# Kernel optimization log

Measured on AMD Instinct MI355X. Metric: run time of the kernel, lower is better.

Reference implementation:

```python
import jax, jax.numpy as jnp
import numpy as np

D_MODEL = 512; D_STATE = 64; D_CONV = 4; HEADDIM = 64
D_INNER = 2 * D_MODEL              # expand=2
NHEADS = D_INNER // HEADDIM        # 16
CONV_DIM = D_INNER + 2 * D_STATE   # 1152
D_IN_PROJ = 2 * D_INNER + 2 * D_STATE + NHEADS  # 2192
BATCH, SEQ = 4, 1024
EPS = 1e-5


def rmsnorm(x, w):
    return x * jax.lax.rsqrt(jnp.mean(x * x, axis=-1, keepdims=True) + EPS) * w


def mamba2(u, in_w, conv_w, conv_b, dt_bias, A_log, D, gnorm_w, out_w):
    b, l, _ = u.shape
    zxbcdt = u @ in_w.T                                  # [b,l,D_IN_PROJ]
    z = zxbcdt[..., :D_INNER]
    xBC = zxbcdt[..., D_INNER:D_INNER + CONV_DIM]
    dt = jax.nn.softplus(zxbcdt[..., -NHEADS:] + dt_bias)  # [b,l,h]
    # causal depthwise conv1d (kernel D_CONV, left pad) + silu
    pad = jnp.pad(xBC, ((0, 0), (D_CONV - 1, 0), (0, 0)))
    acc = conv_b
    for k in range(D_CONV):
        acc = acc + pad[:, k:k + l, :] * conv_w[:, k]
    xBC = jax.nn.silu(acc)
    x = xBC[..., :D_INNER].reshape(b, l, NHEADS, HEADDIM)
    Bm = xBC[..., D_INNER:D_INNER + D_STATE]             # [b,l,n]
    Cm = xBC[..., D_INNER + D_STATE:]                    # [b,l,n]
    A = -jnp.exp(A_log)                                  # [h]
    decay = jnp.exp(dt * A)                              # [b,l,h]
    dtx = dt[..., None] * x                              # [b,l,h,p]

    def step(h, inp):
        dec, dx, Bt, Ct = inp
        h = h * dec[:, :, None, None] + dx[..., None] * Bt[:, None, None, :]
        y = jnp.einsum('bhpn,bn->bhp', h, Ct)
        return h, y

    h0 = jnp.zeros((b, NHEADS, HEADDIM, D_STATE), u.dtype)
    _, ys = jax.lax.scan(step, h0, (decay.transpose(1, 0, 2),
                                    dtx.transpose(1, 0, 2, 3),
                                    Bm.transpose(1, 0, 2),
                                    Cm.transpose(1, 0, 2)))
    y = ys.transpose(1, 0, 2, 3) + x * D[None, None, :, None]  # [b,l,h,p]
    y = y.reshape(b, l, D_INNER)
    y = rmsnorm(y * jax.nn.silu(z), gnorm_w)             # gated RMSNorm
    return y @ out_w.T


def setup_inputs() -> dict:
    key = jax.random.key(0)
    ks = iter(jax.random.split(key, 32))
    def rn(shape, scale=0.02):
        return jax.random.normal(next(ks), shape, dtype=jnp.float32) * scale
    inp = {
        'x': jax.random.normal(next(ks), (BATCH, SEQ, D_MODEL), dtype=jnp.float32),
        'norm_w': jnp.ones((D_MODEL,), jnp.float32),
    }
    for p in ('f', 'b'):
        inp[p + '_in_w'] = rn((D_IN_PROJ, D_MODEL))
        inp[p + '_conv_w'] = rn((CONV_DIM, D_CONV), 0.1)
        inp[p + '_conv_b'] = jnp.zeros((CONV_DIM,), jnp.float32)
        inp[p + '_dt_bias'] = rn((NHEADS,), 0.5)
        inp[p + '_A_log'] = jnp.log(jnp.arange(1, NHEADS + 1, dtype=jnp.float32))
        inp[p + '_D'] = jnp.ones((NHEADS,), jnp.float32)
        inp[p + '_gnorm_w'] = jnp.ones((D_INNER,), jnp.float32)
        inp[p + '_out_w'] = rn((D_MODEL, D_INNER))
    inp['proj_w'] = rn((D_MODEL, 2 * D_MODEL))
    return inp


def reference(x, norm_w,
              f_in_w, f_conv_w, f_conv_b, f_dt_bias, f_A_log, f_D, f_gnorm_w, f_out_w,
              b_in_w, b_conv_w, b_conv_b, b_dt_bias, b_A_log, b_D, b_gnorm_w, b_out_w,
              proj_w):
    h = rmsnorm(x, norm_w)
    fo = mamba2(h, f_in_w, f_conv_w, f_conv_b, f_dt_bias, f_A_log, f_D, f_gnorm_w, f_out_w)
    bo = jnp.flip(mamba2(jnp.flip(h, 1), b_in_w, b_conv_w, b_conv_b, b_dt_bias,
                         b_A_log, b_D, b_gnorm_w, b_out_w), 1)
    return x + jnp.concatenate([fo, bo], axis=-1) @ proj_w.T
```

## Files before the change

kernel.cpp:

```cpp
#include <hip/hip_runtime.h>
#include <math.h>

typedef unsigned short u16;
typedef __bf16  bf16x8 __attribute__((ext_vector_type(8)));
typedef float   f32x4  __attribute__((ext_vector_type(4)));
typedef unsigned short u16x8 __attribute__((ext_vector_type(8)));

#define SEQ 1024
#define MR  4096
#define DIP 2192
#define DI  1024
#define NH  16
#define CD  1152
#define NCH 32
#define CT  32
#define NIN (DIP*512)
#define NOUT (512*1024)
#define ZROW 4384

__device__ __forceinline__ u16 f2bf(float f) {
  union { float f; unsigned u; } v; v.f = f;
  unsigned r = v.u + 0x7FFFu + ((v.u >> 16) & 1u);
  return (u16)(r >> 16);
}
__device__ __forceinline__ float bf2f(u16 h) {
  union { unsigned u; float f; } v; v.u = ((unsigned)h) << 16; return v.f;
}
__device__ __forceinline__ void splitbf(float v, u16& h, u16& l) {
  h = f2bf(v); l = f2bf(v - bf2f(h));
}
__device__ __forceinline__ float sigm(float x){ return 1.f/(1.f+__expf(-x)); }

__device__ __forceinline__ unsigned packbf(float v) {
  u16 hh, ll; splitbf(v, hh, ll);
  return (unsigned)hh | ((unsigned)ll << 16);
}
__device__ __forceinline__ float unpackf(unsigned w) {
  return bf2f((u16)w) + bf2f((u16)(w >> 16));
}

__device__ __forceinline__ void unpack8(const unsigned* p, bf16x8& H, bf16x8& L) {
  uint4 a = *(const uint4*)p, b = *(const uint4*)(p+4);
  u16x8 hu, lu;
  hu[0]=(u16)a.x; lu[0]=(u16)(a.x>>16);
  hu[1]=(u16)a.y; lu[1]=(u16)(a.y>>16);
  hu[2]=(u16)a.z; lu[2]=(u16)(a.z>>16);
  hu[3]=(u16)a.w; lu[3]=(u16)(a.w>>16);
  hu[4]=(u16)b.x; lu[4]=(u16)(b.x>>16);
  hu[5]=(u16)b.y; lu[5]=(u16)(b.y>>16);
  hu[6]=(u16)b.z; lu[6]=(u16)(b.z>>16);
  hu[7]=(u16)b.w; lu[7]=(u16)(b.w>>16);
  H = __builtin_bit_cast(bf16x8, hu);
  L = __builtin_bit_cast(bf16x8, lu);
}
__device__ __forceinline__ void unpack8s(const unsigned* p, int stride, bf16x8& H, bf16x8& L) {
  u16x8 hu, lu;
  #pragma unroll
  for (int jj=0;jj<8;jj++){ unsigned w = p[(size_t)jj*stride]; hu[jj]=(u16)w; lu[jj]=(u16)(w>>16); }
  H = __builtin_bit_cast(bf16x8, hu);
  L = __builtin_bit_cast(bf16x8, lu);
}

__device__ __forceinline__ void gl16(const u16* g, u16* l) {
  __builtin_amdgcn_global_load_lds((const __attribute__((address_space(1))) void*)g,
                                   (__attribute__((address_space(3))) void*)l,
                                   16, 0, 0);
}

__global__ __launch_bounds__(256) void cast_all(
  const float* __restrict__ f_in, const float* __restrict__ b_in,
  const float* __restrict__ f_out, const float* __restrict__ b_out,
  const float* __restrict__ proj,
  u16* __restrict__ H, u16* __restrict__ L, unsigned* __restrict__ wpk)
{
  int i = blockIdx.x*256 + threadIdx.x;
  constexpr int TOT = 2*NIN + 3*NOUT;
  if (i >= TOT) return;
  float v;
  if (i < NIN)               v = f_in[i];
  else if (i < 2*NIN)        v = b_in[i-NIN];
  else if (i < 2*NIN+NOUT)   v = f_out[i-2*NIN];
  else if (i < 2*NIN+2*NOUT) v = b_out[i-2*NIN-NOUT];
  else                       v = proj[i-2*NIN-2*NOUT];
  if (i < 2*NIN) {
    u16 hh, ll; splitbf(v, hh, ll);
    H[i] = hh; L[i] = ll;
  } else {
    wpk[i - 2*NIN] = packbf(v);
  }
}

__global__ __launch_bounds__(256) void wcomb(
  const unsigned* __restrict__ wpk,
  u16* __restrict__ Wch, u16* __restrict__ Wcl)
{
  int d = blockIdx.z;
  int o0 = blockIdx.x*64, p0 = blockIdx.y*128;
  int wv = threadIdx.x>>6, lane = threadIdx.x&63;
  int quad = lane>>4, l16 = lane&15;
  const unsigned* owp = wpk + (size_t)d*NOUT;
  const unsigned* pjp = wpk + 2*(size_t)NOUT;
  int pc = p0 + wv*32;
  f32x4 acc[4][2] = {};
  for (int kt=0; kt<512; kt+=32) {
    bf16x8 ahf[4], alf[4], bhf[2], blf[2];
    #pragma unroll
    for (int ia=0; ia<4; ia++)
      unpack8(pjp + (size_t)(o0 + 16*ia + l16)*1024 + d*512 + kt + quad*8, ahf[ia], alf[ia]);
    #pragma unroll
    for (int jb=0; jb<2; jb++)
      unpack8s(owp + (size_t)(kt + quad*8)*1024 + pc + 16*jb + l16, 1024, bhf[jb], blf[jb]);
    #pragma unroll
    for (int ia=0; ia<4; ia++)
      #pragma unroll
      for (int jb=0; jb<2; jb++) {
        f32x4 t = __builtin_amdgcn_mfma_f32_16x16x32_bf16(ahf[ia], blf[jb], acc[ia][jb], 0,0,0);
        t       = __builtin_amdgcn_mfma_f32_16x16x32_bf16(alf[ia], bhf[jb], t,           0,0,0);
        acc[ia][jb] = __builtin_amdgcn_mfma_f32_16x16x32_bf16(ahf[ia], bhf[jb], t,       0,0,0);
      }
  }
  #pragma unroll
  for (int ia=0; ia<4; ia++)
  #pragma unroll
  for (int jb=0; jb<2; jb++)
  #pragma unroll
  for (int r=0; r<4; r++) {
    int o = o0 + 16*ia + quad*4 + r;
    int p = pc + 16*jb + l16;
    u16 hh, ll; splitbf(acc[ia][jb][r], hh, ll);
    Wch[(size_t)d*NOUT + (size_t)o*1024 + p] = hh;
    Wcl[(size_t)d*NOUT + (size_t)o*1024 + p] = ll;
  }
}

__global__ __launch_bounds__(256) void rmsnorm_x(const float* __restrict__ x,
                                                 const float* __restrict__ w,
                                                 u16* __restrict__ hbh,
                                                 u16* __restrict__ hbl){
  int m = blockIdx.x, tid = threadIdx.x;
  const float* xr = x + (size_t)m*512;
  float2 v = *(const float2*)&xr[tid*2];
  float ss = v.x*v.x + v.y*v.y;
  #pragma unroll
  for (int off=32; off; off>>=1) ss += __shfl_xor(ss, off, 64);
  __shared__ float red[4];
  if ((tid&63)==0) red[tid>>6] = ss;
  __syncthreads();
  float total = red[0]+red[1]+red[2]+red[3];
  float rs = rsqrtf(total*(1.f/512.f) + 1e-5f);
  float2 w2 = *(const float2*)&w[tid*2];
  u16 h0,l0,h1,l1;
  splitbf(v.x*rs*w2.x, h0, l0);
  splitbf(v.y*rs*w2.y, h1, l1);
  *(unsigned*)&hbh[(size_t)m*512 + tid*2] = (unsigned)h0 | ((unsigned)h1<<16);
  *(unsigned*)&hbl[(size_t)m*512 + tid*2] = (unsigned)l0 | ((unsigned)l1<<16);
}

__global__ __launch_bounds__(256) void gemm_in(
    const u16* __restrict__ Ah, const u16* __restrict__ Al,
    const u16* __restrict__ Wh, const u16* __restrict__ Wl,
    float* __restrict__ C0)
{
  constexpr int K = 512;
  constexpr int N = DIP;
  __shared__ __align__(16) u16 sAh[128*32];
  __shared__ __align__(16) u16 sAl[128*32];
  __shared__ __align__(16) u16 sBh[128*32];
  __shared__ __align__(16) u16 sBl[128*32];
  const int tid = threadIdx.x;
  const int dir = blockIdx.z;
  const int m0 = blockIdx.x * 128;
  const int n0 = blockIdx.y * 128;
  const int lane = tid & 63;
  const int wid  = tid >> 6;
  const u16* wh_p = Wh + (size_t)dir*NIN;
  const u16* wl_p = Wl + (size_t)dir*NIN;
  const int j0 = wid, j1 = wid + 4;
  const int cp = lane & 3;
  auto goff = [&](int j, bool isB)->size_t {
    int row = 16*j + (lane>>2);
    int s = (row>>1) & 3;
    int kc = (cp ^ s) * 8;
    int grow;
    if (!isB) {
      grow = m0 + row;
      if (dir) grow = (grow & ~1023) + (1023 - (grow & 1023));
    } else {
      grow = n0 + row;
      if (grow >= N) grow = N-1;
    }
    return (size_t)grow*K + kc;
  };
  const size_t a0 = goff(j0,false), a1 = goff(j1,false);
  const size_t b0 = goff(j0,true),  b1 = goff(j1,true);
  const int wm = (wid & 1) * 64;
  const int wn = (wid >> 1) * 64;
  const int quad = lane >> 4;
  const int l16  = lane & 15;
  const int qx = quad ^ ((l16>>1)&3);
  const int baseA = ((wm + l16)*4 + qx)*8;
  const int baseB = ((wn + l16)*4 + qx)*8;
  f32x4 acc[4][4] = {};
  for (int kt = 0; kt < K; kt += 32) {
    __syncthreads();
    gl16(Ah + a0 + kt, &sAh[j0*512]);  gl16(Ah + a1 + kt, &sAh[j1*512]);
    gl16(Al + a0 + kt, &sAl[j0*512]);  gl16(Al + a1 + kt, &sAl[j1*512]);
    gl16(wh_p + b0 + kt, &sBh[j0*512]);  gl16(wh_p + b1 + kt, &sBh[j1*512]);
    gl16(wl_p + b0 + kt, &sBl[j0*512]);  gl16(wl_p + b1 + kt, &sBl[j1*512]);
    __syncthreads();
    bf16x8 ah[4], al[4], bh[4], bl[4];
    #pragma unroll
    for (int i=0;i<4;i++) {
      ah[i] = *(const bf16x8*)&sAh[baseA + i*512];
      al[i] = *(const bf16x8*)&sAl[baseA + i*512];
    }
    #pragma unroll
    for (int j=0;j<4;j++) {
      bh[j] = *(const bf16x8*)&sBh[baseB + j*512];
      bl[j] = *(const bf16x8*)&sBl[baseB + j*512];
    }
    #pragma unroll
    for (int i=0;i<4;i++)
      #pragma unroll
      for (int j=0;j<4;j++) {
        f32x4 t = __builtin_amdgcn_mfma_f32_16x16x32_bf16(ah[i], bl[j], acc[i][j], 0,0,0);
        t       = __builtin_amdgcn_mfma_f32_16x16x32_bf16(al[i], bh[j], t,         0,0,0);
        acc[i][j] = __builtin_amdgcn_mfma_f32_16x16x32_bf16(ah[i], bh[j], t,       0,0,0);
      }
  }
  #pragma unroll
  for (int i=0;i<4;i++)
  #pragma unroll
  for (int j=0;j<4;j++)
  #pragma unroll
  for (int r=0;r<4;r++) {
    int mo = m0 + wm + i*16 + quad*4 + r;
    int no = n0 + wn + j*16 + l16;
    if (no < N) C0[((size_t)dir*MR + mo)*DIP + no] = acc[i][j][r];
  }
}

__global__ __launch_bounds__(512) void gemm_final(
    const u16* __restrict__ zt, const u16* __restrict__ Wch, const u16* __restrict__ Wcl,
    const float* __restrict__ X0, float* __restrict__ out)
{
  __shared__ __align__(16) u16 sAh[64*32];
  __shared__ __align__(16) u16 sAl[64*32];
  __shared__ __align__(16) u16 sBh[128*32];
  __shared__ __align__(16) u16 sBl[128*32];
  const int tid = threadIdx.x;
  const int lane = tid & 63, wid = tid >> 6;
  const int m0 = blockIdx.x * 64, n0 = blockIdx.y * 128;
  const int cp = lane & 3;
  const int quad = lane >> 4, l16 = lane & 15;
  const int wm = (wid & 1) * 32;
  const int wn = (wid >> 1) * 32;
  const int qx = quad ^ ((l16>>1)&3);
  const int baseA = ((wm + l16)*4 + qx)*8;
  const int baseB = ((wn + l16)*4 + qx)*8;
  f32x4 acc[2][2] = {};
  const int jb0 = (wid-4)*2, jb1 = jb0+1;
  for (int dir=0; dir<2; ++dir) {
    size_t aoff=0, boff0=0, boff1=0;
    if (wid < 4) {
      int row = 16*wid + (lane>>2);
      int s = (row>>1) & 3;
      int kc = (cp ^ s) * 8;
      int grow = m0 + row;
      if (dir) grow = (grow & ~1023) + (1023 - (grow & 1023));
      aoff = (size_t)(dir*MR + grow)*ZROW + kc;
    } else {
      int row0 = 16*jb0 + (lane>>2);
      int s0 = (row0>>1) & 3;
      boff0 = (size_t)dir*NOUT + (size_t)(n0 + row0)*1024 + (cp ^ s0)*8;
      int row1 = 16*jb1 + (lane>>2);
      int s1 = (row1>>1) & 3;
      boff1 = (size_t)dir*NOUT + (size_t)(n0 + row1)*1024 + (cp ^ s1)*8;
    }
    for (int kt = 0; kt < 1024; kt += 32) {
      __syncthreads();
      if (wid < 4) {
        gl16(zt + 2048 + aoff + kt, &sAh[wid*512]);
        gl16(zt + 3072 + aoff + kt, &sAl[wid*512]);
      } else {
        gl16(Wch + boff0 + kt, &sBh[jb0*512]);
        gl16(Wch + boff1 + kt, &sBh[jb1*512]);
        gl16(Wcl + boff0 + kt, &sBl[jb0*512]);
        gl16(Wcl + boff1 + kt, &sBl[jb1*512]);
      }
      __syncthreads();
      bf16x8 ah[2], al[2], bh[2], bl[2];
      #pragma unroll
      for (int i=0;i<2;i++) {
        ah[i] = *(const bf16x8*)&sAh[baseA + i*512];
        al[i] = *(const bf16x8*)&sAl[baseA + i*512];
      }
      #pragma unroll
      for (int j=0;j<2;j++) {
        bh[j] = *(const bf16x8*)&sBh[baseB + j*512];
        bl[j] = *(const bf16x8*)&sBl[baseB + j*512];
      }
      #pragma unroll
      for (int i=0;i<2;i++)
        #pragma unroll
        for (int j=0;j<2;j++) {
          f32x4 t = __builtin_amdgcn_mfma_f32_16x16x32_bf16(ah[i], bl[j], acc[i][j], 0,0,0);
          t       = __builtin_amdgcn_mfma_f32_16x16x32_bf16(al[i], bh[j], t,         0,0,0);
          acc[i][j] = __builtin_amdgcn_mfma_f32_16x16x32_bf16(ah[i], bh[j], t,       0,0,0);
        }
    }
  }
  #pragma unroll
  for (int i=0;i<2;i++)
  #pragma unroll
  for (int j=0;j<2;j++)
  #pragma unroll
  for (int r=0;r<4;r++) {
    int mo = m0 + wm + 16*i + quad*4 + r;
    int no = n0 + wn + 16*j + l16;
    out[(size_t)mo*512 + no] = acc[i][j][r] + X0[(size_t)mo*512 + no];
  }
}

__global__ __launch_bounds__(320) void conv_dt(
  const float* __restrict__ Z,
  const float* __restrict__ f_cw, const float* __restrict__ f_cb,
  const float* __restrict__ b_cw, const float* __restrict__ b_cb,
  const float* __restrict__ f_dtb, const float* __restrict__ b_dtb,
  unsigned* __restrict__ xconv,
  unsigned* __restrict__ Bc, unsigned* __restrict__ Cc,
  float* __restrict__ dtq)
{
  int bm = blockIdx.x;
  int dir = bm >> 12;
  int t = bm & 1023;
  const float* cw  = dir ? b_cw : f_cw;
  const float* cb  = dir ? b_cb : f_cb;
  const float* dtb = dir ? b_dtb : f_dtb;
  int tid = threadIdx.x;
  if (tid < 288) {
    int c0 = tid*4;
    const float* zbase = Z + (size_t)(bm-3)*DIP + 1024 + c0;
    float4 w0 = *(const float4*)&cw[c0*4];
    float4 w1 = *(const float4*)&cw[(c0+1)*4];
    float4 w2 = *(const float4*)&cw[(c0+2)*4];
    float4 w3 = *(const float4*)&cw[(c0+3)*4];
    float4 z0 = {0,0,0,0}, z1 = {0,0,0,0}, z2 = {0,0,0,0};
    float4 z3 = *(const float4*)(zbase + 3*(size_t)DIP);
    if (t >= 3) {
      z0 = *(const float4*)(zbase);
      z1 = *(const float4*)(zbase + (size_t)DIP);
      z2 = *(const float4*)(zbase + 2*(size_t)DIP);
    } else {
      if (t >= 1) z2 = *(const float4*)(zbase + 2*(size_t)DIP);
      if (t >= 2) z1 = *(const float4*)(zbase + (size_t)DIP);
    }
    float4 a = *(const float4*)&cb[c0];
    a.x += z0.x*w0.x + z1.x*w0.y + z2.x*w0.z + z3.x*w0.w;
    a.y += z0.y*w1.x + z1.y*w1.y + z2.y*w1.z + z3.y*w1.w;
    a.z += z0.z*w2.x + z1.z*w2.y + z2.z*w2.z + z3.z*w2.w;
    a.w += z0.w*w3.x + z1.w*w3.y + z2.w*w3.z + z3.w*w3.w;
    float4 v;
    v.x = a.x * sigm(a.x); v.y = a.y * sigm(a.y);
    v.z = a.z * sigm(a.z); v.w = a.w * sigm(a.w);
    uint4 pv;
    pv.x = packbf(v.x); pv.y = packbf(v.y);
    pv.z = packbf(v.z); pv.w = packbf(v.w);
    if (c0 < 1024)      *(uint4*)&xconv[(size_t)bm*DI + c0] = pv;
    else if (c0 < 1088) *(uint4*)&Bc[(size_t)bm*64 + (c0-1024)] = pv;
    else                *(uint4*)&Cc[(size_t)bm*64 + (c0-1088)] = pv;
  }
  if (tid < NH) {
    float dtraw = Z[(size_t)bm*DIP + 2176 + tid] + dtb[tid];
    float dt = (dtraw > 20.f) ? dtraw : log1pf(__expf(dtraw));
    dtq[(size_t)bm*NH + tid] = dt;
  }
}

__global__ __launch_bounds__(256) void scan_mfma(
  const float* __restrict__ dtq, const unsigned* __restrict__ xconv,
  const unsigned* __restrict__ Bc, const unsigned* __restrict__ Cc,
  const float* __restrict__ f_Al, const float* __restrict__ b_Al,
  float* __restrict__ yraw, float* __restrict__ cumdec, float* __restrict__ S)
{
  __shared__ __align__(16) u16 sMh[4][32*40];
  __shared__ __align__(16) u16 sMl[4][32*40];
  __shared__ float scum[4][32];
  __shared__ float sdt[4][32];
  int bx = blockIdx.x;
  int hq = bx & 3, chunk = (bx>>2)&(NCH-1), dirb = bx>>7;
  int w = threadIdx.x >> 6, lane = threadIdx.x & 63;
  int h = hq*4 + w;
  int base_row = dirb*1024 + chunk*CT;
  const int quad = lane >> 4, l16 = lane & 15;
  const float* Al = (dirb >= 4) ? b_Al : f_Al;
  float A = -__expf(Al[h]);
  float dtl = 0.f, cum = 0.f;
  if (lane < 32) { dtl = dtq[(size_t)(base_row + lane)*16 + h]; cum = dtl; }
  #pragma unroll
  for (int off=1; off<32; off<<=1) {
    int src = (lane >= off) ? lane-off : lane;
    float o = __shfl(cum, src);
    if (lane >= off && lane < 32) cum += o;
  }
  if (lane < 32) {
    sdt[w][lane]  = dtl;
    scum[w][lane] = cum;
    cumdec[(size_t)(base_row + lane)*16 + h] = __expf(A*cum);
  }
  bf16x8 chf[2][2], clf[2][2], bhf[2][2], blf[2][2];
  #pragma unroll
  for (int i=0;i<2;i++)
  #pragma unroll
  for (int kk=0;kk<2;kk++) {
    unpack8(Cc + (size_t)(base_row + 16*i + l16)*64 + kk*32 + quad*8, chf[i][kk], clf[i][kk]);
    unpack8(Bc + (size_t)(base_row + 16*i + l16)*64 + kk*32 + quad*8, bhf[i][kk], blf[i][kk]);
  }
  f32x4 g[2][2];
  __builtin_amdgcn_s_setprio(1);
  #pragma unroll
  for (int i=0;i<2;i++)
  #pragma unroll
  for (int j=0;j<2;j++) {
    f32x4 acc = {};
    #pragma unroll
    for (int kk=0;kk<2;kk++) {
      acc = __builtin_amdgcn_mfma_f32_16x16x32_bf16(chf[i][kk], blf[j][kk], acc, 0,0,0);
      acc = __builtin_amdgcn_mfma_f32_16x16x32_bf16(clf[i][kk], bhf[j][kk], acc, 0,0,0);
      acc = __builtin_amdgcn_mfma_f32_16x16x32_bf16(chf[i][kk], bhf[j][kk], acc, 0,0,0);
    }
    g[i][j] = acc;
  }
  __builtin_amdgcn_s_setprio(0);
  float ctt[2][4];
  #pragma unroll
  for (int i=0;i<2;i++)
  #pragma unroll
  for (int r=0;r<4;r++) ctt[i][r] = scum[w][16*i + quad*4 + r];
  #pragma unroll
  for (int j=0;j<2;j++) {
    int s = 16*j + l16;
    float cts = scum[w][s];
    float dts = sdt[w][s];
    #pragma unroll
    for (int i=0;i<2;i++)
    #pragma unroll
    for (int r=0;r<4;r++) {
      int t = 16*i + quad*4 + r;
      float mv = (s <= t) ? g[i][j][r] * __expf(A*(ctt[i][r]-cts)) * dts : 0.f;
      u16 hh, ll; splitbf(mv, hh, ll);
      sMh[w][t*40 + s] = hh;
      sMl[w][t*40 + s] = ll;
    }
  }
  bf16x8 xhf[4], xlf[4];
  const unsigned* xp = xconv + (size_t)(base_row + quad*8)*1024 + h*64 + l16;
  #pragma unroll
  for (int jp=0;jp<4;jp++) unpack8s(xp + 16*jp, 1024, xhf[jp], xlf[jp]);
  bf16x8 mhf[2], mlf[2];
  #pragma unroll
  for (int i=0;i<2;i++) {
    mhf[i] = *(const bf16x8*)&sMh[w][(16*i + l16)*40 + quad*8];
    mlf[i] = *(const bf16x8*)&sMl[w][(16*i + l16)*40 + quad*8];
  }
  __builtin_amdgcn_s_setprio(1);
  #pragma unroll
  for (int i=0;i<2;i++)
  #pragma unroll
  for (int jp=0;jp<4;jp++) {
    f32x4 acc = {};
    acc = __builtin_amdgcn_mfma_f32_16x16x32_bf16(mhf[i], xlf[jp], acc, 0,0,0);
    acc = __builtin_amdgcn_mfma_f32_16x16x32_bf16(mlf[i], xhf[jp], acc, 0,0,0);
    acc = __builtin_amdgcn_mfma_f32_16x16x32_bf16(mhf[i], xhf[jp], acc, 0,0,0);
    #pragma unroll
    for (int r=0;r<4;r++)
      yraw[(size_t)(base_row + 16*i + quad*4 + r)*1024 + h*64 + 16*jp + l16] = acc[r];
  }
  __builtin_amdgcn_s_setprio(0);
  float wv[8];
  float ct31 = scum[w][31];
  #pragma unroll
  for (int jj=0;jj<8;jj++) {
    int s = quad*8 + jj;
    wv[jj] = sdt[w][s] * __expf(A*(ct31 - scum[w][s]));
  }
  bf16x8 wbh[4], wbl[4];
  #pragma unroll
  for (int j2=0;j2<4;j2++) {
    u16x8 hu, lu; u16 hh, ll;
    #pragma unroll
    for (int jj=0;jj<8;jj++) {
      float b = unpackf(Bc[(size_t)(base_row + quad*8 + jj)*64 + 16*j2 + l16]);
      splitbf(wv[jj]*b, hh, ll); hu[jj]=hh; lu[jj]=ll;
    }
    wbh[j2] = __builtin_bit_cast(bf16x8, hu);
    wbl[j2] = __builtin_bit_cast(bf16x8, lu);
  }
  size_t inst = ((size_t)(dirb*16+h)*NCH + chunk)*4096;
  __builtin_amdgcn_s_setprio(1);
  #pragma unroll
  for (int mp=0;mp<4;mp++)
  #pragma unroll
  for (int j2=0;j2<4;j2++) {
    f32x4 acc = {};
    acc = __builtin_amdgcn_mfma_f32_16x16x32_bf16(xhf[mp], wbl[j2], acc, 0,0,0);
    acc = __builtin_amdgcn_mfma_f32_16x16x32_bf16(xlf[mp], wbh[j2], acc, 0,0,0);
    acc = __builtin_amdgcn_mfma_f32_16x16x32_bf16(xhf[mp], wbh[j2], acc, 0,0,0);
    #pragma unroll
    for (int r=0;r<4;r++)
      S[inst + (size_t)(16*mp + quad*4 + r)*64 + 16*j2 + l16] = acc[r];
  }
  __builtin_amdgcn_s_setprio(0);
}

__global__ __launch_bounds__(256) void scan_comb(
  const float* __restrict__ cumdec, float* __restrict__ S)
{
  int ih = blockIdx.x >> 4;
  int sub = blockIdx.x & 15;
  int dirb = ih >> 4, h = ih & 15;
  int elem = sub*256 + threadIdx.x;
  size_t base = (size_t)ih*NCH*4096 + elem;
  float hr = 0.f;
  for (int c=0;c<NCH;c++) {
    float P = cumdec[((size_t)(dirb*1024 + c*CT + CT-1))*16 + h];
    float s = S[base + c*4096];
    S[base + c*4096] = __builtin_bit_cast(float, packbf(hr));
    hr = fmaf(hr, P, s);
  }
}

__global__ __launch_bounds__(1024) void scan_y2_gate(
  const unsigned* __restrict__ Cc, const float* __restrict__ cumdec,
  const float* __restrict__ S, const float* __restrict__ yraw,
  const unsigned* __restrict__ xconv, const float* Z, u16* zt,
  const float* __restrict__ f_D, const float* __restrict__ b_D,
  const float* __restrict__ f_gw, const float* __restrict__ b_gw)
{
  __shared__ float vbuf[32][1028];
  __shared__ float red[32][17];
  __shared__ float rsb[32];
  int bx = blockIdx.x;
  int chunk = bx & (NCH-1), dirb = bx >> 5;
  int w = threadIdx.x >> 6, lane = threadIdx.x & 63;
  int h = w;
  int dir = dirb >> 2;
  int row0 = dirb*1024 + chunk*CT;
  const int quad = lane>>4, l16 = lane&15;
  const float* Dp  = dir ? b_D  : f_D;
  const float* gwp = dir ? b_gw : f_gw;
  float Dv = Dp[h];

  f32x4 acc[2][4] = {};
  float at[2][4] = {};
  if (chunk > 0) {
    size_t inst = ((size_t)(dirb*16+h)*NCH + chunk)*4096;
    #pragma unroll
    for (int i=0;i<2;i++)
    #pragma unroll
    for (int r=0;r<4;r++)
      at[i][r] = cumdec[(size_t)(row0 + 16*i + quad*4 + r)*16 + h];
    bf16x8 chf[2][2], clf[2][2];
    #pragma unroll
    for (int i=0;i<2;i++)
    #pragma unroll
    for (int kk=0;kk<2;kk++)
      unpack8(Cc + (size_t)(row0 + 16*i + l16)*64 + kk*32 + quad*8, chf[i][kk], clf[i][kk]);
    const unsigned* Sp = (const unsigned*)S;
    __builtin_amdgcn_s_setprio(1);
    #pragma unroll
    for (int j=0;j<4;j++) {
      bf16x8 hhf[2], hlf[2];
      #pragma unroll
      for (int kk=0;kk<2;kk++)
        unpack8(Sp + inst + (size_t)(16*j + l16)*64 + kk*32 + quad*8, hhf[kk], hlf[kk]);
      #pragma unroll
      for (int i=0;i<2;i++) {
        f32x4 a2 = acc[i][j];
        #pragma unroll
        for (int kk=0;kk<2;kk++) {
          a2 = __builtin_amdgcn_mfma_f32_16x16x32_bf16(chf[i][kk], hlf[kk], a2, 0,0,0);
          a2 = __builtin_amdgcn_mfma_f32_16x16x32_bf16(clf[i][kk], hhf[kk], a2, 0,0,0);
          a2 = __builtin_amdgcn_mfma_f32_16x16x32_bf16(chf[i][kk], hhf[kk], a2, 0,0,0);
        }
        acc[i][j] = a2;
      }
    }
    __builtin_amdgcn_s_setprio(0);
  }
  float pss[2][4] = {};
  #pragma unroll
  for (int i=0;i<2;i++)
  #pragma unroll
  for (int r=0;r<4;r++) {
    int t = 16*i + quad*4 + r;
    size_t g = (size_t)(row0 + t);
    #pragma unroll
    for (int j=0;j<4;j++) {
      int c = h*64 + 16*j + l16;
      float yv = yraw[g*1024 + c];
      float xv = unpackf(xconv[g*1024 + c]);
      float zv = Z[g*DIP + c];
      float v = (yv + xv*Dv + at[i][r]*acc[i][j][r]) * (zv * sigm(zv));
      vbuf[t][c] = v;
      pss[i][r] += v*v;
    }
  }
  #pragma unroll
  for (int i=0;i<2;i++)
  #pragma unroll
  for (int r=0;r<4;r++) {
    float s2 = pss[i][r];
    s2 += __shfl_xor(s2, 1, 64);
    s2 += __shfl_xor(s2, 2, 64);
    s2 += __shfl_xor(s2, 4, 64);
    s2 += __shfl_xor(s2, 8, 64);
    if (l16 == 0) red[16*i + quad*4 + r][w] = s2;
  }
  __syncthreads();
  if (threadIdx.x < 32) {
    int t = threadIdx.x;
    float tot = 0.f;
    #pragma unroll
    for (int ww=0; ww<16; ww++) tot += red[t][ww];
    rsb[t] = rsqrtf(tot*(1.f/1024.f) + 1e-5f);
  }
  __syncthreads();
  #pragma unroll
  for (int i=0;i<2;i++)
  #pragma unroll
  for (int r=0;r<4;r++) {
    int t = 16*i + quad*4 + r;
    size_t g = (size_t)(row0 + t);
    float rs = rsb[t];
    #pragma unroll
    for (int j=0;j<4;j++) {
      int c = h*64 + 16*j + l16;
      float o = vbuf[t][c] * rs * gwp[c];
      u16 hh, ll; splitbf(o, hh, ll);
      zt[g*ZROW + 2048 + c] = hh;
      zt[g*ZROW + 3072 + c] = ll;
    }
  }
}

extern "C" void kernel_launch(void* const* d_in, const int* in_sizes, int n_in,
                              void* d_out, int out_size, void* d_ws, size_t ws_size,
                              hipStream_t stream)
{
  const float* x        = (const float*)d_in[0];
  const float* norm_w   = (const float*)d_in[1];
  const float* f_in_w   = (const float*)d_in[2];
  const float* f_conv_w = (const float*)d_in[3];
  const float* f_conv_b = (const float*)d_in[4];
  const float* f_dt_bias= (const float*)d_in[5];
  const float* f_A_log  = (const float*)d_in[6];
  const float* f_D      = (const float*)d_in[7];
  const float* f_gw     = (const float*)d_in[8];
  const float* f_out_w  = (const float*)d_in[9];
  const float* b_in_w   = (const float*)d_in[10];
  const float* b_conv_w = (const float*)d_in[11];
  const float* b_conv_b = (const float*)d_in[12];
  const float* b_dt_bias= (const float*)d_in[13];
  const float* b_A_log  = (const float*)d_in[14];
  const float* b_D      = (const float*)d_in[15];
  const float* b_gw     = (const float*)d_in[16];
  const float* b_out_w  = (const float*)d_in[17];
  const float* proj_w   = (const float*)d_in[18];

  char* ws = (char*)d_ws;
  size_t off = 0;
  auto alloc = [&](size_t bytes)->char* {
    char* p = ws + off; off = (off + bytes + 255) & ~(size_t)255; return p;
  };
  u16*   hbh   = (u16*)  alloc((size_t)MR*512*2);
  u16*   hbl   = (u16*)  alloc((size_t)MR*512*2);
  u16*   wH    = (u16*)  alloc(2*(size_t)NIN*2);
  u16*   wL    = (u16*)  alloc(2*(size_t)NIN*2);
  unsigned* wpk = (unsigned*)alloc(3*(size_t)NOUT*4);
  u16*   Wch   = (u16*)  alloc(2*(size_t)NOUT*2);
  u16*   Wcl   = (u16*)  alloc(2*(size_t)NOUT*2);
  float* Z     = (float*)alloc(2*(size_t)MR*DIP*4);
  unsigned* xconv = (unsigned*)alloc(2*(size_t)MR*DI*4);
  unsigned* Bc    = (unsigned*)alloc(2*(size_t)MR*64*4);
  unsigned* Cc    = (unsigned*)alloc(2*(size_t)MR*64*4);
  float* dtq   = (float*)alloc(2*(size_t)MR*NH*4);
  float* cumdec= (float*)alloc(2*(size_t)MR*NH*4);
  float* S     = (float*)alloc((size_t)4096*4096*4);
  float* yraw  = (float*)alloc(2*(size_t)MR*DI*4);
  u16* wih = wH;  u16* wil = wL;

  constexpr int TOT = 2*NIN + 3*NOUT;
  cast_all<<<(TOT+255)/256,256,0,stream>>>(f_in_w, b_in_w, f_out_w, b_out_w, proj_w,
                                           wH, wL, wpk);
  wcomb<<<dim3(8,8,2),256,0,stream>>>(wpk, Wch, Wcl);

  rmsnorm_x<<<MR,256,0,stream>>>(x, norm_w, hbh, hbl);
  gemm_in<<<dim3(32,18,2),256,0,stream>>>(hbh, hbl, wih, wil, Z);
  conv_dt<<<2*MR,320,0,stream>>>(Z, f_conv_w, f_conv_b, b_conv_w, b_conv_b,
                                 f_dt_bias, b_dt_bias, xconv, Bc, Cc, dtq);
  scan_mfma<<<1024,256,0,stream>>>(dtq, xconv, Bc, Cc, f_A_log, b_A_log,
                                   yraw, cumdec, S);
  scan_comb<<<2048,256,0,stream>>>(cumdec, S);
  scan_y2_gate<<<256,1024,0,stream>>>(Cc, cumdec, S, yraw, xconv, Z, (u16*)Z,
                                      f_D, b_D, f_gw, b_gw);
  gemm_final<<<dim3(64,4),512,0,stream>>>((u16*)Z, Wch, Wcl, x, (float*)d_out);
}
```

Baseline: 380.4 us.

## Split final GEMM K-loop across directions into separate blocks with add kernel

The final projection GEMM used to loop over both scan directions inside one 512-thread block. It now launches one 256-thread block per direction via blockIdx.z, doubling the grid from 256 to 512 blocks. The forward direction writes output plus residual, and the backward direction writes a partial into a reused yraw buffer. A new elementwise kernel then adds the two. This raises parallelism and occupancy for a small grid, at the cost of an extra launch and an extra 8MB read/write pass.

```diff
diff --git a/kernel.cpp b/kernel.cpp
--- a/kernel.cpp
+++ b/kernel.cpp
@@ -240,86 +240,97 @@
   }
 }
 
-__global__ __launch_bounds__(512) void gemm_final(
+__global__ __launch_bounds__(256) void gemm_final(
     const u16* __restrict__ zt, const u16* __restrict__ Wch, const u16* __restrict__ Wcl,
-    const float* __restrict__ X0, float* __restrict__ out)
-{
+    const float* __restrict__ X0, float* __restrict__ out, float* __restrict__ Pb)
+{
+  constexpr int K = 1024;
   __shared__ __align__(16) u16 sAh[64*32];
   __shared__ __align__(16) u16 sAl[64*32];
   __shared__ __align__(16) u16 sBh[128*32];
   __shared__ __align__(16) u16 sBl[128*32];
   const int tid = threadIdx.x;
-  const int lane = tid & 63, wid = tid >> 6;
-  const int m0 = blockIdx.x * 64, n0 = blockIdx.y * 128;
+  const int dir = blockIdx.z;
+  const int m0 = blockIdx.x * 64;
+  const int n0 = blockIdx.y * 128;
+  const int lane = tid & 63;
+  const int wid  = tid >> 6;
+  const u16* ah_p = zt + 2048 + (size_t)dir*MR*ZROW;
+  const u16* al_p = zt + 3072 + (size_t)dir*MR*ZROW;
+  const u16* wh_p = Wch + (size_t)dir*NOUT;
+  const u16* wl_p = Wcl + (size_t)dir*NOUT;
   const int cp = lane & 3;
-  const int quad = lane >> 4, l16 = lane & 15;
-  const int wm = (wid & 1) * 32;
-  const int wn = (wid >> 1) * 32;
+  auto goffA = [&](int j)->size_t {
+    int row = 16*j + (lane>>2);
+    int s = (row>>1) & 3;
+    int kc = (cp ^ s) * 8;
+    int grow = m0 + row;
+    if (dir) grow = (grow & ~1023) + (1023 - (grow & 1023));
+    return (size_t)grow*ZROW + kc;
+  };
+  auto goffB = [&](int j)->size_t {
+    int row = 16*j + (lane>>2);
+    int s = (row>>1) & 3;
+    int kc = (cp ^ s) * 8;
+    return (size_t)(n0 + row)*1024 + kc;
+  };
+  const size_t a0 = goffA(wid);
+  const size_t b0 = goffB(wid), b1 = goffB(wid+4);
+  const int quad = lane >> 4;
+  const int l16  = lane & 15;
   const int qx = quad ^ ((l16>>1)&3);
-  const int baseA = ((wm + l16)*4 + qx)*8;
-  const int baseB = ((wn + l16)*4 + qx)*8;
-  f32x4 acc[2][2] = {};
-  const int jb0 = (wid-4)*2, jb1 = jb0+1;
-  for (int dir=0; dir<2; ++dir) {
-    size_t aoff=0, boff0=0, boff1=0;
-    if (wid < 4) {
-      int row = 16*wid + (lane>>2);
-      int s = (row>>1) & 3;
-      int kc = (cp ^ s) * 8;
-      int grow = m0 + row;
-      if (dir) grow = (grow & ~1023) + (1023 - (grow & 1023));
-      aoff = (size_t)(dir*MR + grow)*ZROW + kc;
-    } else {
-      int row0 = 16*jb0 + (lane>>2);
-      int s0 = (row0>>1) & 3;
-      boff0 = (size_t)dir*NOUT + (size_t)(n0 + row0)*1024 + (cp ^ s0)*8;
-      int row1 = 16*jb1 + (lane>>2);
-      int s1 = (row1>>1) & 3;
-      boff1 = (size_t)dir*NOUT + (size_t)(n0 + row1)*1024 + (cp ^ s1)*8;
-    }
-    for (int kt = 0; kt < 1024; kt += 32) {
-      __syncthreads();
-      if (wid < 4) {
-        gl16(zt + 2048 + aoff + kt, &sAh[wid*512]);
-        gl16(zt + 3072 + aoff + kt, &sAl[wid*512]);
-      } else {
-        gl16(Wch + boff0 + kt, &sBh[jb0*512]);
-        gl16(Wch + boff1 + kt, &sBh[jb1*512]);
-        gl16(Wcl + boff0 + kt, &sBl[jb0*512]);
-        gl16(Wcl + boff1 + kt, &sBl[jb1*512]);
-      }
-      __syncthreads();
-      bf16x8 ah[2], al[2], bh[2], bl[2];
-      #pragma unroll
-      for (int i=0;i<2;i++) {
-        ah[i] = *(const bf16x8*)&sAh[baseA + i*512];
-        al[i] = *(const bf16x8*)&sAl[baseA + i*512];
-      }
+  const int baseA = (l16*4 + qx)*8;
+  const int baseB = ((wid*32 + l16)*4 + qx)*8;
+  f32x4 acc[4][2] = {};
+  for (int kt = 0; kt < K; kt += 32) {
+    __syncthreads();
+    gl16(ah_p + a0 + kt, &sAh[wid*512]);
+    gl16(al_p + a0 + kt, &sAl[wid*512]);
+    gl16(wh_p + b0 + kt, &sBh[wid*512]);  gl16(wh_p + b1 + kt, &sBh[(wid+4)*512]);
+    gl16(wl_p + b0 + kt, &sBl[wid*512]);  gl16(wl_p + b1 + kt, &sBl[(wid+4)*512]);
+    __syncthreads();
+    bf16x8 ah[4], al[4], bh[2], bl[2];
+    #pragma unroll
+    for (int i=0;i<4;i++) {
+      ah[i] = *(const bf16x8*)&sAh[baseA + i*512];
+      al[i] = *(const bf16x8*)&sAl[baseA + i*512];
+    }
+    #pragma unroll
+    for (int j=0;j<2;j++) {
+      bh[j] = *(const bf16x8*)&sBh[baseB + j*512];
+      bl[j] = *(const bf16x8*)&sBl[baseB + j*512];
+    }
+    #pragma unroll
+    for (int i=0;i<4;i++)
       #pragma unroll
       for (int j=0;j<2;j++) {
-        bh[j] = *(const bf16x8*)&sBh[baseB + j*512];
-        bl[j] = *(const bf16x8*)&sBl[baseB + j*512];
+        f32x4 t = __builtin_amdgcn_mfma_f32_16x16x32_bf16(ah[i], bl[j], acc[i][j], 0,0,0);
+        t       = __builtin_amdgcn_mfma_f32_16x16x32_bf16(al[i], bh[j], t,         0,0,0);
+        acc[i][j] = __builtin_amdgcn_mfma_f32_16x16x32_bf16(ah[i], bh[j], t,       0,0,0);
       }
-      #pragma unroll
-      for (int i=0;i<2;i++)
-        #pragma unroll
-        for (int j=0;j<2;j++) {
-          f32x4 t = __builtin_amdgcn_mfma_f32_16x16x32_bf16(ah[i], bl[j], acc[i][j], 0,0,0);
-          t       = __builtin_amdgcn_mfma_f32_16x16x32_bf16(al[i], bh[j], t,         0,0,0);
-          acc[i][j] = __builtin_amdgcn_mfma_f32_16x16x32_bf16(ah[i], bh[j], t,       0,0,0);
-        }
-    }
-  }
-  #pragma unroll
-  for (int i=0;i<2;i++)
+  }
+  #pragma unroll
+  for (int i=0;i<4;i++)
   #pragma unroll
   for (int j=0;j<2;j++)
   #pragma unroll
   for (int r=0;r<4;r++) {
-    int mo = m0 + wm + 16*i + quad*4 + r;
-    int no = n0 + wn + 16*j + l16;
-    out[(size_t)mo*512 + no] = acc[i][j][r] + X0[(size_t)mo*512 + no];
-  }
+    int mo = m0 + i*16 + quad*4 + r;
+    int no = n0 + wid*32 + j*16 + l16;
+    float v = acc[i][j][r];
+    if (dir == 0) out[(size_t)mo*512 + no] = v + X0[(size_t)mo*512 + no];
+    else          Pb[(size_t)mo*512 + no] = v;
+  }
+}
+
+__global__ __launch_bounds__(256) void addout(float* __restrict__ out,
+                                              const float* __restrict__ Pb)
+{
+  size_t i = ((size_t)blockIdx.x*256 + threadIdx.x)*4;
+  float4 a = *(const float4*)&out[i];
+  float4 b = *(const float4*)&Pb[i];
+  a.x += b.x; a.y += b.y; a.z += b.z; a.w += b.w;
+  *(float4*)&out[i] = a;
 }
 
 __global__ __launch_bounds__(320) void conv_dt(
@@ -689,6 +700,7 @@
   float* S     = (float*)alloc((size_t)4096*4096*4);
   float* yraw  = (float*)alloc(2*(size_t)MR*DI*4);
   u16* wih = wH;  u16* wil = wL;
+  float* Pb = yraw;
 
   constexpr int TOT = 2*NIN + 3*NOUT;
   cast_all<<<(TOT+255)/256,256,0,stream>>>(f_in_w, b_in_w, f_out_w, b_out_w, proj_w,
@@ -704,5 +716,6 @@
   scan_comb<<<2048,256,0,stream>>>(cumdec, S);
   scan_y2_gate<<<256,1024,0,stream>>>(Cc, cumdec, S, yraw, xconv, Z, (u16*)Z,
                                       f_D, b_D, f_gw, b_gw);
-  gemm_final<<<dim3(64,4),512,0,stream>>>((u16*)Z, Wch, Wcl, x, (float*)d_out);
-}
+  gemm_final<<<dim3(64,4,2),256,0,stream>>>((u16*)Z, Wch, Wcl, x, (float*)d_out, Pb);
+  addout<<<2048,256,0,stream>>>((float*)d_out, Pb);
+}
```

New measurement: 367.0 us. 3.5% less time.
